# Kernel tuning notes

Measured on AMD Instinct MI355X. Metric: run time of the kernel, lower is better.

The kernel has to match this reference:

```python
import jax, jax.numpy as jnp
import numpy as np
from jax import lax

# Static problem configuration (SAModule(ratio=0.25, r=0.2, MLP([35,64,64,128])))
B, N, C_IN = 8, 4096, 32
RATIO, R, K = 0.25, 0.2, 64   # K == max_num_neighbors
M = int(N * RATIO)            # centroids per cloud after FPS
NEG = -1e10


def setup_inputs() -> dict:
    key = jax.random.key(0)
    ks = jax.random.split(key, 6)
    x = jax.random.normal(ks[0], (B * N, C_IN), jnp.float32)
    pos = jax.random.uniform(ks[1], (B * N, 3), jnp.float32)  # unit cube -> r=0.2 balls are non-trivial
    batch = jnp.repeat(jnp.arange(B, dtype=jnp.int32), N)
    def lin(k, fan_in, fan_out):
        return jax.random.normal(k, (fan_in, fan_out), jnp.float32) * (1.0 / np.sqrt(fan_in))
    W1 = lin(ks[2], C_IN + 3, 64); b1 = jnp.zeros((64,), jnp.float32)
    W2 = lin(ks[3], 64, 64);       b2 = jnp.zeros((64,), jnp.float32)
    W3 = lin(ks[4], 64, 128);      b3 = jnp.zeros((128,), jnp.float32)
    return {"x": x, "pos": pos, "batch": batch,
            "W1": W1, "b1": b1, "W2": W2, "b2": b2, "W3": W3, "b3": b3}


def _fps_one(p):
    """Farthest-point sampling on one cloud p:[N,3] -> idx:[M] (deterministic start at 0)."""
    def body(carry, _):
        dmin, last = carry
        d = jnp.sum((p - p[last]) ** 2, axis=-1)         # [N] sq-dist to last picked point
        dmin = jnp.minimum(dmin, d)
        nxt = jnp.argmax(dmin).astype(jnp.int32)
        return (dmin, nxt), nxt
    init = (jnp.full((N,), 1e10, jnp.float32), jnp.int32(0))
    _, rest = lax.scan(body, init, None, length=M - 1)
    return jnp.concatenate([jnp.zeros((1,), jnp.int32), rest])


def _sa_one(p, xb, ib, W1, b1, W2, b2, W3, b3):
    """Radius ball-query + PointNetConv (gather -> MLP -> masked scatter-max) on one cloud."""
    ctr = p[ib]                                              # [M,3] sampled centroids
    d2 = jnp.sum((ctr[:, None, :] - p[None, :, :]) ** 2, -1)  # [M,N]
    negd, nbr = lax.top_k(-d2, K)                            # K nearest per centroid
    valid = (-negd) <= R * R                                 # inside-ball mask [M,K]
    xj = xb[nbr]                                             # [M,K,C_IN] gathered features
    rel = p[nbr] - ctr[:, None, :]                           # [M,K,3] relative positions
    h = jnp.concatenate([xj, rel], axis=-1)                  # message input [x_j, pos_j - pos_i]
    h = jax.nn.relu(h @ W1 + b1)
    h = jax.nn.relu(h @ W2 + b2)
    h = h @ W3 + b3                                          # plain last layer (PyG MLP plain_last)
    h = jnp.where(valid[..., None], h, NEG)
    return jnp.max(h, axis=1)                                # max aggregation -> [M,128]


def reference(x, pos, batch, W1, b1, W2, b2, W3, b3):
    pos3 = pos.reshape(B, N, 3)
    x3 = x.reshape(B, N, C_IN)
    idx = jax.vmap(_fps_one)(pos3)                           # [B,M]
    conv = lambda p, xb, ib: _sa_one(p, xb, ib, W1, b1, W2, b2, W3, b3)
    x_out = jax.vmap(conv)(pos3, x3, idx)                    # [B,M,128]
    pos_out = jnp.take_along_axis(pos3, idx[..., None], axis=1)  # [B,M,3]
    batch_out = jnp.repeat(jnp.arange(B, dtype=batch.dtype), M)
    return x_out.reshape(B * M, -1), pos_out.reshape(B * M, 3), batch_out
```

## Files before the change

kernel.cpp:

```cpp
#include <hip/hip_runtime.h>
#include <hip/hip_bf16.h>

#define BB 8
#define NN 4096
#define CIN 32
#define MM 1024
#define KNB 64
#define CAND 1024
#define FPS_T 512
#define FPS_PPT 8
#define ROWS 72

typedef __attribute__((ext_vector_type(8))) short  short8;
typedef __attribute__((ext_vector_type(4))) float  f32x4;

__device__ __forceinline__ float sq3(float dx, float dy, float dz) {
    return __fadd_rn(__fadd_rn(__fmul_rn(dx, dx), __fmul_rn(dy, dy)), __fmul_rn(dz, dz));
}

__device__ __forceinline__ unsigned short f2bf(float v) {
    union { __hip_bfloat16 b; unsigned short u; } cv;
    cv.b = __float2bfloat16(v);
    return cv.u;
}
__device__ __forceinline__ float bf2f(unsigned short u) {
    union { unsigned short u; __hip_bfloat16 b; } cv;
    cv.u = u;
    return __bfloat162float(cv.b);
}

static __device__ __forceinline__ f32x4 mfma16(short8 a, short8 b, f32x4 c) {
    return __builtin_amdgcn_mfma_f32_16x16x32_bf16(a, b, c, 0, 0, 0);
}

template<int CTRL>
__device__ __forceinline__ unsigned long long dpp_maxkey(unsigned long long k) {
    unsigned int lo = (unsigned int)k;
    unsigned int hi = (unsigned int)(k >> 32);
    unsigned int nlo = (unsigned int)__builtin_amdgcn_update_dpp((int)lo, (int)lo, CTRL, 0xF, 0xF, false);
    unsigned int nhi = (unsigned int)__builtin_amdgcn_update_dpp((int)hi, (int)hi, CTRL, 0xF, 0xF, false);
    unsigned long long nk = ((unsigned long long)nhi << 32) | (unsigned long long)nlo;
    return nk > k ? nk : k;
}

__global__ __launch_bounds__(256) void prep_kernel(
    const float* __restrict__ W1, const float* __restrict__ W2,
    const float* __restrict__ W3, unsigned short* __restrict__ wf)
{
    int gid = blockIdx.x * 256 + threadIdx.x;
    const float* W; int K, Ncol, base, slot;
    if (gid < 1024)      { W = W1; K = 35; Ncol = 64;  base = 0;     slot = gid; }
    else if (gid < 2048) { W = W2; K = 64; Ncol = 64;  base = 8192;  slot = gid - 1024; }
    else                 { W = W3; K = 64; Ncol = 128; base = 16384; slot = gid - 2048; }
    int lane = slot & 63, h = (slot >> 6) & 1, kstep = (slot >> 7) & 1, tile = slot >> 8;
    int col = tile * 16 + (lane & 15), quad = lane >> 4;
#pragma unroll
    for (int j = 0; j < 8; ++j) {
        int k = kstep * 32 + quad * 8 + j;
        float wv = (k < K) ? W[k * Ncol + col] : 0.0f;
        unsigned short hi = f2bf(wv);
        unsigned short v = h ? f2bf(wv - bf2f(hi)) : hi;
        wf[base + slot * 8 + j] = v;
    }
}

__global__ __launch_bounds__(FPS_T) void fps_kernel(
    const float* __restrict__ pos, int* __restrict__ idx_ws, float* __restrict__ out)
{
    const int b = blockIdx.x;
    const int t = threadIdx.x;
    __shared__ float4 plds4[NN];
    __shared__ int    chosen[MM];
    __shared__ __align__(16) unsigned long long part[2][FPS_T / 64];

    const float* P = pos + (size_t)b * NN * 3;
    for (int i = t; i < NN; i += FPS_T) {
        float4 v;
        v.x = P[3 * i]; v.y = P[3 * i + 1]; v.z = P[3 * i + 2]; v.w = 0.0f;
        plds4[i] = v;
    }
    if (t == 0) chosen[0] = 0;
    __syncthreads();

    float px[FPS_PPT], py[FPS_PPT], pz[FPS_PPT], dmin[FPS_PPT];
#pragma unroll
    for (int s = 0; s < FPS_PPT; ++s) {
        int i = t + FPS_T * s;
        float4 v = plds4[i];
        px[s] = v.x; py[s] = v.y; pz[s] = v.z;
        dmin[s] = 1e10f;
    }

    int win = 0;
    for (int it = 1; it < MM; ++it) {
        float4 wc = plds4[win];
        const float lx = wc.x, ly = wc.y, lz = wc.z;
        float bv = -1.0f;
        int   bi = 0;
#pragma unroll
        for (int s = 0; s < FPS_PPT; ++s) {
            float dx = px[s] - lx, dy = py[s] - ly, dz = pz[s] - lz;
            float d  = sq3(dx, dy, dz);
            float dm = fminf(dmin[s], d);
            dmin[s] = dm;
            if (dm > bv) { bv = dm; bi = t + FPS_T * s; }
        }
        unsigned long long k =
            ((unsigned long long)__float_as_uint(bv) << 32) | (unsigned int)(~bi);
        k = dpp_maxkey<0x111>(k);
        k = dpp_maxkey<0x112>(k);
        k = dpp_maxkey<0x114>(k);
        k = dpp_maxkey<0x118>(k);
        k = dpp_maxkey<0x142>(k);
        k = dpp_maxkey<0x143>(k);
        if ((t & 63) == 63) part[it & 1][t >> 6] = k;
        __syncthreads();
        const ulonglong2* pp = (const ulonglong2*)&part[it & 1][0];
        ulonglong2 p01 = pp[0], p23 = pp[1], p45 = pp[2], p67 = pp[3];
        unsigned long long km = p01.x;
        km = p01.y > km ? p01.y : km;
        km = p23.x > km ? p23.x : km;
        km = p23.y > km ? p23.y : km;
        km = p45.x > km ? p45.x : km;
        km = p45.y > km ? p45.y : km;
        km = p67.x > km ? p67.x : km;
        km = p67.y > km ? p67.y : km;
        win = (int)(~(unsigned int)km);
        if (t == 0) chosen[it] = win;
    }
    __syncthreads();

    for (int m = t; m < MM; m += FPS_T) {
        int mi = chosen[m];
        idx_ws[b * MM + m] = mi;
        const int PO = BB * MM * 128;
        const int BO = PO + BB * MM * 3;
        int row = b * MM + m;
        float4 c = plds4[mi];
        out[PO + 3 * row + 0] = c.x;
        out[PO + 3 * row + 1] = c.y;
        out[PO + 3 * row + 2] = c.z;
        out[BO + row] = (float)b;
    }
}

__global__ __launch_bounds__(256, 3) void sa_kernel(
    const float* __restrict__ x, const float* __restrict__ pos,
    const int* __restrict__ idx_ws, const unsigned short* __restrict__ wf,
    const float* __restrict__ b1, const float* __restrict__ b2,
    const float* __restrict__ b3, float* __restrict__ out)
{
    const int bm = blockIdx.x;
    const int b  = bm >> 10;
    const int t  = threadIdx.x;
    const int w    = t >> 6;
    const int lane = t & 63;

    __shared__ unsigned short HA[2 * 64 * ROWS];
    __shared__ unsigned short HB[2 * 64 * ROWS];
    __shared__ float cd2[CAND];
    __shared__ int   cid[CAND];
    __shared__ int   cnt;
    __shared__ int   sel[KNB];
    __shared__ float red[4][128];

    const float R2 = (float)(0.2 * 0.2);
    const float* P = pos + (size_t)b * NN * 3;
    const int ci = idx_ws[bm];

    if (t == 0) cnt = 0;
    {
        short8 z = {};
        short8* z8 = (short8*)HA;
        for (int i = t; i < (2 * 64 * ROWS) / 8; i += 256) z8[i] = z;
    }

    const float cx = P[3 * ci], cy = P[3 * ci + 1], cz = P[3 * ci + 2];

    for (int i = t; i < NN; i += 256) {
        float dx = P[3 * i] - cx, dy = P[3 * i + 1] - cy, dz = P[3 * i + 2] - cz;
        float d2 = sq3(dx, dy, dz);
        if (d2 <= R2) {
            int p = atomicAdd(&cnt, 1);
            if (p < CAND) { cd2[p] = d2; cid[p] = i; }
        }
    }
    __syncthreads();
    const int n = min(cnt, CAND);
    const int V = min(n, KNB);

    for (int i = t; i < n; i += 256) {
        float di = cd2[i];
        int   ii = cid[i];
        int rank = 0;
        for (int j = 0; j < n; ++j) {
            float dj = cd2[j];
            int   ij = cid[j];
            rank += (dj < di || (dj == di && ij < ii)) ? 1 : 0;
        }
        if (rank < KNB) sel[rank] = ii;
    }
    __syncthreads();

    {
        const int row  = 16 * w + (lane & 15);
        const int prt  = lane >> 4;
        if (row < V) {
            int g = b * NN + sel[row];
            const float4* xr = (const float4*)(x + (size_t)g * CIN + prt * 8);
            float4 v0 = xr[0], v1 = xr[1];
            float vv[8] = {v0.x, v0.y, v0.z, v0.w, v1.x, v1.y, v1.z, v1.w};
            short8 hv, lv;
#pragma unroll
            for (int j = 0; j < 8; ++j) {
                unsigned short h = f2bf(vv[j]);
                hv[j] = (short)h;
                lv[j] = (short)f2bf(vv[j] - bf2f(h));
            }
            *(short8*)(HA + row * ROWS + prt * 8) = hv;
            *(short8*)(HA + 64 * ROWS + row * ROWS + prt * 8) = lv;
            if (prt == 0) {
                int g2 = sel[row];
#pragma unroll
                for (int c = 0; c < 3; ++c) {
                    float cc = (c == 0) ? cx : (c == 1) ? cy : cz;
                    float rv = P[3 * g2 + c] - cc;
                    unsigned short h = f2bf(rv);
                    HA[row * ROWS + 32 + c] = h;
                    HA[64 * ROWS + row * ROWS + 32 + c] = f2bf(rv - bf2f(h));
                }
            }
        }
    }

    const int m16  = lane & 15;
    const int quad = lane >> 4;
    const int arow = 16 * w + m16;
    const short8* wf8 = (const short8*)wf;

    {
        short8 aH[2], aL[2];
        aH[0] = *(const short8*)(HA + arow * ROWS + quad * 8);
        aH[1] = *(const short8*)(HA + arow * ROWS + 32 + quad * 8);
        aL[0] = *(const short8*)(HA + 64 * ROWS + arow * ROWS + quad * 8);
        aL[1] = *(const short8*)(HA + 64 * ROWS + arow * ROWS + 32 + quad * 8);
#pragma unroll
        for (int tile = 0; tile < 4; ++tile) {
            f32x4 acc = {};
#pragma unroll
            for (int ks = 0; ks < 2; ++ks) {
                short8 bH = wf8[((tile * 2 + ks) * 2 + 0) * 64 + lane];
                short8 bL = wf8[((tile * 2 + ks) * 2 + 1) * 64 + lane];
                acc = mfma16(aH[ks], bH, acc);
                acc = mfma16(aH[ks], bL, acc);
                acc = mfma16(aL[ks], bH, acc);
            }
            int col = tile * 16 + m16;
            float bb = b1[col];
#pragma unroll
            for (int i = 0; i < 4; ++i) {
                int grow = 16 * w + quad * 4 + i;
                float v = fmaxf(acc[i] + bb, 0.0f);
                unsigned short h = f2bf(v);
                HB[grow * ROWS + col] = h;
                HB[64 * ROWS + grow * ROWS + col] = f2bf(v - bf2f(h));
            }
        }
    }

    {
        short8 aH[2], aL[2];
        aH[0] = *(const short8*)(HB + arow * ROWS + quad * 8);
        aH[1] = *(const short8*)(HB + arow * ROWS + 32 + quad * 8);
        aL[0] = *(const short8*)(HB + 64 * ROWS + arow * ROWS + quad * 8);
        aL[1] = *(const short8*)(HB + 64 * ROWS + arow * ROWS + 32 + quad * 8);
#pragma unroll
        for (int tile = 0; tile < 4; ++tile) {
            f32x4 acc = {};
#pragma unroll
            for (int ks = 0; ks < 2; ++ks) {
                short8 bH = wf8[1024 + ((tile * 2 + ks) * 2 + 0) * 64 + lane];
                short8 bL = wf8[1024 + ((tile * 2 + ks) * 2 + 1) * 64 + lane];
                acc = mfma16(aH[ks], bH, acc);
                acc = mfma16(aH[ks], bL, acc);
                acc = mfma16(aL[ks], bH, acc);
            }
            int col = tile * 16 + m16;
            float bb = b2[col];
#pragma unroll
            for (int i = 0; i < 4; ++i) {
                int grow = 16 * w + quad * 4 + i;
                float v = fmaxf(acc[i] + bb, 0.0f);
                unsigned short h = f2bf(v);
                HA[grow * ROWS + col] = h;
                HA[64 * ROWS + grow * ROWS + col] = f2bf(v - bf2f(h));
            }
        }
    }

    {
        short8 aH[2], aL[2];
        aH[0] = *(const short8*)(HA + arow * ROWS + quad * 8);
        aH[1] = *(const short8*)(HA + arow * ROWS + 32 + quad * 8);
        aL[0] = *(const short8*)(HA + 64 * ROWS + arow * ROWS + quad * 8);
        aL[1] = *(const short8*)(HA + 64 * ROWS + arow * ROWS + 32 + quad * 8);
#pragma unroll
        for (int tile = 0; tile < 8; ++tile) {
            f32x4 acc = {};
#pragma unroll
            for (int ks = 0; ks < 2; ++ks) {
                short8 bH = wf8[2048 + ((tile * 2 + ks) * 2 + 0) * 64 + lane];
                short8 bL = wf8[2048 + ((tile * 2 + ks) * 2 + 1) * 64 + lane];
                acc = mfma16(aH[ks], bH, acc);
                acc = mfma16(aH[ks], bL, acc);
                acc = mfma16(aL[ks], bH, acc);
            }
            float mv = -1e10f;
#pragma unroll
            for (int i = 0; i < 4; ++i) {
                int grow = 16 * w + quad * 4 + i;
                float v = (grow < V) ? acc[i] : -1e10f;
                mv = fmaxf(mv, v);
            }
            mv = fmaxf(mv, __shfl_xor(mv, 16));
            mv = fmaxf(mv, __shfl_xor(mv, 32));
            if (lane < 16) red[w][tile * 16 + lane] = mv;
        }
    }
    __syncthreads();

    if (t < 128) {
        float v = fmaxf(fmaxf(red[0][t], red[1][t]), fmaxf(red[2][t], red[3][t]));
        out[(size_t)bm * 128 + t] = v + b3[t];
    }
}

extern "C" void kernel_launch(void* const* d_in, const int* in_sizes, int n_in,
                              void* d_out, int out_size, void* d_ws, size_t ws_size,
                              hipStream_t stream) {
    const float* x   = (const float*)d_in[0];
    const float* pos = (const float*)d_in[1];
    const float* W1 = (const float*)d_in[3];
    const float* b1 = (const float*)d_in[4];
    const float* W2 = (const float*)d_in[5];
    const float* b2 = (const float*)d_in[6];
    const float* W3 = (const float*)d_in[7];
    const float* b3 = (const float*)d_in[8];
    float* out    = (float*)d_out;
    int*   idx_ws = (int*)d_ws;
    unsigned short* wf = (unsigned short*)((char*)d_ws + 32768);

    hipLaunchKernelGGL(prep_kernel, dim3(16), dim3(256), 0, stream, W1, W2, W3, wf);
    hipLaunchKernelGGL(fps_kernel, dim3(BB), dim3(FPS_T), 0, stream, pos, idx_ws, out);
    hipLaunchKernelGGL(sa_kernel, dim3(BB * MM), dim3(256), 0, stream,
                       x, pos, idx_ws, wf, b1, b2, b3, out);
}
```

Baseline: 876.4 us.

## Halve FPS block size and alias MLP LDS buffers to raise SA occupancy

The FPS kernel now uses 256 threads with 16 points each, so its cross-wave reduction covers 4 partials instead of 8 and each barrier involves fewer waves. The SA kernel drops its second shared-memory activation buffer and writes layer-1 outputs back into the input buffer in place. Instead of zeroing the whole buffer it clears only the padding columns per row, and the launch-bound occupancy hint rises from 3 to 4 blocks. The in-place reuse relies on barriers between reading layer-1 inputs and writing its outputs; if those are missing the results are wrong. Fewer FPS threads also means less parallelism per distance update in that serial loop.

Result: faster. 799.7 us (-8.8%).

```diff
diff --git a/kernel.cpp b/kernel.cpp
--- a/kernel.cpp
+++ b/kernel.cpp
@@ -7,8 +7,8 @@
 #define MM 1024
 #define KNB 64
 #define CAND 1024
-#define FPS_T 512
-#define FPS_PPT 8
+#define FPS_T 256
+#define FPS_PPT 16
 #define ROWS 72
 
 typedef __attribute__((ext_vector_type(8))) short  short8;
@@ -116,15 +116,10 @@
         if ((t & 63) == 63) part[it & 1][t >> 6] = k;
         __syncthreads();
         const ulonglong2* pp = (const ulonglong2*)&part[it & 1][0];
-        ulonglong2 p01 = pp[0], p23 = pp[1], p45 = pp[2], p67 = pp[3];
-        unsigned long long km = p01.x;
-        km = p01.y > km ? p01.y : km;
-        km = p23.x > km ? p23.x : km;
-        km = p23.y > km ? p23.y : km;
-        km = p45.x > km ? p45.x : km;
-        km = p45.y > km ? p45.y : km;
-        km = p67.x > km ? p67.x : km;
-        km = p67.y > km ? p67.y : km;
+        ulonglong2 p01 = pp[0], p23 = pp[1];
+        unsigned long long ka = p01.x > p01.y ? p01.x : p01.y;
+        unsigned long long kb = p23.x > p23.y ? p23.x : p23.y;
+        unsigned long long km = ka > kb ? ka : kb;
         win = (int)(~(unsigned int)km);
         if (t == 0) chosen[it] = win;
     }
@@ -144,7 +139,7 @@
     }
 }
 
-__global__ __launch_bounds__(256, 3) void sa_kernel(
+__global__ __launch_bounds__(256, 4) void sa_kernel(
     const float* __restrict__ x, const float* __restrict__ pos,
     const int* __restrict__ idx_ws, const unsigned short* __restrict__ wf,
     const float* __restrict__ b1, const float* __restrict__ b2,
@@ -157,7 +152,6 @@
     const int lane = t & 63;
 
     __shared__ unsigned short HA[2 * 64 * ROWS];
-    __shared__ unsigned short HB[2 * 64 * ROWS];
     __shared__ float cd2[CAND];
     __shared__ int   cid[CAND];
     __shared__ int   cnt;
@@ -169,11 +163,7 @@
     const int ci = idx_ws[bm];
 
     if (t == 0) cnt = 0;
-    {
-        short8 z = {};
-        short8* z8 = (short8*)HA;
-        for (int i = t; i < (2 * 64 * ROWS) / 8; i += 256) z8[i] = z;
-    }
+    __syncthreads();
 
     const float cx = P[3 * ci], cy = P[3 * ci + 1], cz = P[3 * ci + 2];
 
@@ -203,8 +193,11 @@
     __syncthreads();
 
     {
-        const int row  = 16 * w + (lane & 15);
-        const int prt  = lane >> 4;
+        const int row = 16 * w + (lane & 15);
+        const int prt = lane >> 4;
+        short8 z = {};
+        *(short8*)(HA + row * ROWS + 32 + prt * 8) = z;
+        *(short8*)(HA + 64 * ROWS + row * ROWS + 32 + prt * 8) = z;
         if (row < V) {
             int g = b * NN + sel[row];
             const float4* xr = (const float4*)(x + (size_t)g * CIN + prt * 8);
@@ -262,18 +255,18 @@
                 int grow = 16 * w + quad * 4 + i;
                 float v = fmaxf(acc[i] + bb, 0.0f);
                 unsigned short h = f2bf(v);
-                HB[grow * ROWS + col] = h;
-                HB[64 * ROWS + grow * ROWS + col] = f2bf(v - bf2f(h));
+                HA[grow * ROWS + col] = h;
+                HA[64 * ROWS + grow * ROWS + col] = f2bf(v - bf2f(h));
             }
         }
     }
 
     {
         short8 aH[2], aL[2];
-        aH[0] = *(const short8*)(HB + arow * ROWS + quad * 8);
-        aH[1] = *(const short8*)(HB + arow * ROWS + 32 + quad * 8);
-        aL[0] = *(const short8*)(HB + 64 * ROWS + arow * ROWS + quad * 8);
-        aL[1] = *(const short8*)(HB + 64 * ROWS + arow * ROWS + 32 + quad * 8);
+        aH[0] = *(const short8*)(HA + arow * ROWS + quad * 8);
+        aH[1] = *(const short8*)(HA + arow * ROWS + 32 + quad * 8);
+        aL[0] = *(const short8*)(HA + 64 * ROWS + arow * ROWS + quad * 8);
+        aL[1] = *(const short8*)(HA + 64 * ROWS + arow * ROWS + 32 + quad * 8);
 #pragma unroll
         for (int tile = 0; tile < 4; ++tile) {
             f32x4 acc = {};
```
